# Kernel tuning notes

Measured on AMD Instinct MI355X. Metric: run time of the kernel, lower is better.

## Reference

```python
import jax, jax.numpy as jnp
import numpy as np

N_NODES = 50000
N_EDGES = 600000
D_IN = 256    # hidden_lstm
D_GNN = 128   # hidden_gnn
D_OUT = 1     # out_channels


def setup_inputs() -> dict:
    key = jax.random.key(0)
    ks = jax.random.split(key, 8)
    x = jax.random.normal(ks[0], (N_NODES, D_IN), dtype=jnp.float32)
    edge_index = jax.random.randint(ks[1], (2, N_EDGES), 0, N_NODES, dtype=jnp.int32)
    # SAGEConv params: lin_l applied to aggregated neighbors (with bias), lin_r to root
    s_in = 1.0 / np.sqrt(D_IN)
    W_l = jax.random.uniform(ks[2], (D_IN, D_GNN), jnp.float32, -s_in, s_in)
    b_l = jax.random.uniform(ks[3], (D_GNN,), jnp.float32, -s_in, s_in)
    W_r = jax.random.uniform(ks[4], (D_IN, D_GNN), jnp.float32, -s_in, s_in)
    # fc head
    s_g = 1.0 / np.sqrt(D_GNN)
    W_fc = jax.random.uniform(ks[5], (D_GNN, D_OUT), jnp.float32, -s_g, s_g)
    b_fc = jax.random.uniform(ks[6], (D_OUT,), jnp.float32, -s_g, s_g)
    return {"x": x, "edge_index": edge_index, "W_l": W_l, "b_l": b_l,
            "W_r": W_r, "W_fc": W_fc, "b_fc": b_fc}


def reference(x, edge_index, W_l, b_l, W_r, W_fc, b_fc):
    # SAGEConv, aggr='mean': out = lin_l(mean_{j in N(i)} x_j) + lin_r(x_i)
    src = edge_index[0]  # message source
    dst = edge_index[1]  # message target
    n = x.shape[0]
    agg = jax.ops.segment_sum(x[src], dst, num_segments=n)            # [N, D_IN]
    cnt = jax.ops.segment_sum(jnp.ones((src.shape[0], 1), x.dtype), dst,
                              num_segments=n)                         # [N, 1]
    mean = agg / jnp.maximum(cnt, 1.0)
    h = mean @ W_l + b_l + x @ W_r                                    # [N, D_GNN]
    pred = jax.nn.sigmoid(h @ W_fc + b_fc).squeeze()                  # [N]
    return h, pred
```

## Files before the change

kernel.cpp:

```cpp
#include <hip/hip_runtime.h>
#include <hip/hip_bf16.h>
#include <math.h>

#define N_NODES 50000
#define N_EDGES 600000
#define D_IN 256
#define D_GNN 128
#define CAP 32
#define MAX_OVER 8192
#define EB_STRIDE 264

typedef short s16x8 __attribute__((ext_vector_type(8)));
typedef float f32x4 __attribute__((ext_vector_type(4)));

__device__ __forceinline__ unsigned short f2bf(float f) {
  unsigned int u = __float_as_uint(f);
  u += 0x7FFFu + ((u >> 16) & 1u);
  return (unsigned short)(u >> 16);
}

__global__ __launch_bounds__(256) void pack0(
    const float* __restrict__ Wl, const float* __restrict__ Wr,
    ushort* __restrict__ Wcp, int* __restrict__ cursor,
    int* __restrict__ ovcnt) {
  int i = blockIdx.x * 256 + threadIdx.x;
  if (i < N_NODES) cursor[i] = 0;
  if (i == 0) ovcnt[0] = 0;
  if (i < 8192) {
    int q = i & 3, col = (i >> 2) & 255, ks = i >> 10;
    const float* W = (col < 128) ? Wl : Wr;
    int c = col & 127;
    int k0 = ks * 32 + q * 8;
    s16x8 v;
#pragma unroll
    for (int j = 0; j < 8; j++) v[j] = (short)f2bf(W[(k0 + j) * D_GNN + c]);
    *((s16x8*)(Wcp + (size_t)i * 8)) = v;
  }
}

__global__ __launch_bounds__(256, 6) void fused_gemm_fill(
    const float* __restrict__ x, const ushort* __restrict__ Wcp,
    const float* __restrict__ b_l, const int* __restrict__ ei,
    int* __restrict__ cursor, ushort* __restrict__ colp,
    int* __restrict__ ovcnt, int2* __restrict__ over,
    ushort* __restrict__ yb, ushort* __restrict__ yrb) {
  __shared__ ushort eb[16 * EB_STRIDE];
  const int t = threadIdx.x;
  const int n0 = blockIdx.x * 16;
  const int l = t & 63;
  const int w = t >> 6;
  const int lq = l >> 4, l16 = l & 15;

  const int e = blockIdx.x * 256 + t;
  int esrc = 0, edst = 0;
  const bool has_e = (e < N_EDGES);
  if (has_e) {
    esrc = ei[e];
    edst = ei[N_EDGES + e];
  }

  int row = n0 + l16;
  if (row >= N_NODES) row = N_NODES - 1;
  const float* arow = x + (size_t)row * D_IN + lq * 8;

  const ushort* bptr[4];
#pragma unroll
  for (int ct = 0; ct < 4; ct++) {
    int col = w * 64 + ct * 16 + l16;
    bptr[ct] = Wcp + ((size_t)col * 4 + lq) * 8;
  }

  f32x4 acc[4];
#pragma unroll
  for (int ct = 0; ct < 4; ct++) acc[ct] = (f32x4){0.f, 0.f, 0.f, 0.f};

#pragma unroll
  for (int ks = 0; ks < 8; ks++) {
    float4 a0 = *((const float4*)(arow + ks * 32));
    float4 a1 = *((const float4*)(arow + ks * 32 + 4));
    union { s16x8 v; ushort4 u[2]; } ua;
    __hip_bfloat162 h0 = __float22bfloat162_rn(make_float2(a0.x, a0.y));
    __hip_bfloat162 h1 = __float22bfloat162_rn(make_float2(a0.z, a0.w));
    __hip_bfloat162 h2 = __float22bfloat162_rn(make_float2(a1.x, a1.y));
    __hip_bfloat162 h3 = __float22bfloat162_rn(make_float2(a1.z, a1.w));
    ua.u[0].x = ((ushort2*)&h0)->x; ua.u[0].y = ((ushort2*)&h0)->y;
    ua.u[0].z = ((ushort2*)&h1)->x; ua.u[0].w = ((ushort2*)&h1)->y;
    ua.u[1].x = ((ushort2*)&h2)->x; ua.u[1].y = ((ushort2*)&h2)->y;
    ua.u[1].z = ((ushort2*)&h3)->x; ua.u[1].w = ((ushort2*)&h3)->y;
    s16x8 A = ua.v;
#pragma unroll
    for (int ct = 0; ct < 4; ct++) {
      s16x8 B = *((const s16x8*)(bptr[ct] + (size_t)ks * 8192));
      acc[ct] = __builtin_amdgcn_mfma_f32_16x16x32_bf16(A, B, acc[ct], 0, 0, 0);
    }
  }

  int pos = -1;
  if (has_e) pos = atomicAdd(&cursor[edst], 1);

#pragma unroll
  for (int ct = 0; ct < 4; ct++) {
    int col = w * 64 + ct * 16 + l16;
    float bias = (col >= 128) ? b_l[col - 128] : 0.f;
#pragma unroll
    for (int r = 0; r < 4; r++) {
      eb[(lq * 4 + r) * EB_STRIDE + col] = f2bf(acc[ct][r] + bias);
    }
  }

  if (pos >= 0) {
    if (pos < CAP) {
      colp[edst * CAP + pos] = (ushort)esrc;
    } else {
      int o = atomicAdd(ovcnt, 1);
      if (o < MAX_OVER) over[o] = make_int2(edst, esrc);
    }
  }

  __syncthreads();

#pragma unroll
  for (int p = 0; p < 2; p++) {
    int id = p * 256 + t;
    int rl = id >> 5;
    int c8 = (id & 31) * 8;
    int gn = n0 + rl;
    if (gn < N_NODES) {
      s16x8 v = *((const s16x8*)(eb + rl * EB_STRIDE + c8));
      if (c8 < 128)
        *((s16x8*)(yb + (size_t)gn * D_GNN + c8)) = v;
      else
        *((s16x8*)(yrb + (size_t)gn * D_GNN + (c8 - 128))) = v;
    }
  }
}

__global__ __launch_bounds__(256) void gather_pred(
    const int* __restrict__ cursor, const ushort* __restrict__ colp,
    const int* __restrict__ ovcnt, const int2* __restrict__ over,
    const ushort* __restrict__ yb, const ushort* __restrict__ yrb,
    const float* __restrict__ Wfc, const float* __restrict__ bfc,
    float* __restrict__ h, float* __restrict__ pred) {
  const int node = (blockIdx.x * 256 + threadIdx.x) >> 6;
  const int lane = threadIdx.x & 63;
  if (node >= N_NODES) return;
  const int degt = cursor[node];
  const int m = min(degt, CAP);
  float ax = 0.f, ay = 0.f;
  const unsigned int* y32 = (const unsigned int*)yb;

  int c = (lane < m) ? (int)colp[node * CAP + lane] : 0;
  int j = 0;
  for (; j + 4 <= m; j += 4) {
    int s0 = __shfl(c, j), s1 = __shfl(c, j + 1);
    int s2 = __shfl(c, j + 2), s3 = __shfl(c, j + 3);
    unsigned int v0 = y32[(size_t)s0 * 64 + lane];
    unsigned int v1 = y32[(size_t)s1 * 64 + lane];
    unsigned int v2 = y32[(size_t)s2 * 64 + lane];
    unsigned int v3 = y32[(size_t)s3 * 64 + lane];
    ax += __uint_as_float(v0 << 16) + __uint_as_float(v1 << 16) +
          __uint_as_float(v2 << 16) + __uint_as_float(v3 << 16);
    ay += __uint_as_float(v0 & 0xFFFF0000u) + __uint_as_float(v1 & 0xFFFF0000u) +
          __uint_as_float(v2 & 0xFFFF0000u) + __uint_as_float(v3 & 0xFFFF0000u);
  }
  for (; j < m; j++) {
    int s0 = __shfl(c, j);
    unsigned int v0 = y32[(size_t)s0 * 64 + lane];
    ax += __uint_as_float(v0 << 16);
    ay += __uint_as_float(v0 & 0xFFFF0000u);
  }
  if (degt > CAP) {
    int nov = min(ovcnt[0], MAX_OVER);
    for (int k = 0; k < nov; k++) {
      int2 ov = over[k];
      if (ov.x == node) {
        unsigned int v0 = y32[(size_t)ov.y * 64 + lane];
        ax += __uint_as_float(v0 << 16);
        ay += __uint_as_float(v0 & 0xFFFF0000u);
      }
    }
  }

  const float ic = degt > 0 ? 1.f / (float)degt : 0.f;
  unsigned int yrv = ((const unsigned int*)yrb)[(size_t)node * 64 + lane];
  float h0 = ax * ic + __uint_as_float(yrv << 16);
  float h1 = ay * ic + __uint_as_float(yrv & 0xFFFF0000u);
  float2 hv; hv.x = h0; hv.y = h1;
  ((float2*)h)[(size_t)node * 64 + lane] = hv;
  float s = h0 * Wfc[2 * lane] + h1 * Wfc[2 * lane + 1];
#pragma unroll
  for (int off = 32; off > 0; off >>= 1) s += __shfl_down(s, off);
  if (lane == 0) pred[node] = 1.f / (1.f + expf(-(s + bfc[0])));
}

extern "C" void kernel_launch(void* const* d_in, const int* in_sizes, int n_in,
                              void* d_out, int out_size, void* d_ws,
                              size_t ws_size, hipStream_t stream) {
  const float* x   = (const float*)d_in[0];
  const int*   ei  = (const int*)d_in[1];
  const float* Wl  = (const float*)d_in[2];
  const float* bl  = (const float*)d_in[3];
  const float* Wr  = (const float*)d_in[4];
  const float* Wfc = (const float*)d_in[5];
  const float* bfc = (const float*)d_in[6];

  float* out  = (float*)d_out;
  float* h    = out;
  float* pred = out + (size_t)N_NODES * D_GNN;

  ushort* Wcp   = (ushort*)d_ws;
  ushort* yb    = Wcp + 8192 * 8;
  ushort* yrb   = yb + (size_t)N_NODES * D_GNN;
  int*   cursor = (int*)(yrb + (size_t)N_NODES * D_GNN);
  int*   ovcnt  = cursor + N_NODES;
  int2*  over   = (int2*)(ovcnt + 1);
  ushort* colp  = (ushort*)(over + MAX_OVER);

  pack0<<<(N_NODES + 255) / 256, 256, 0, stream>>>(Wl, Wr, Wcp, cursor, ovcnt);

  fused_gemm_fill<<<(N_NODES + 15) / 16, 256, 0, stream>>>(
      x, Wcp, bl, ei, cursor, colp, ovcnt, over, yb, yrb);

  gather_pred<<<(N_NODES * 64 + 255) / 256, 256, 0, stream>>>(
      cursor, colp, ovcnt, over, yb, yrb, Wfc, bfc, h, pred);
}
```

Measured before the change: 192.9 us.

## Make fused GEMM/fill kernel persistent with register-resident weights

Converts the fused GEMM and CSR-fill kernel into a persistent grid of 512 blocks that first grid-strides over edges to do the atomic bucket fill, then loops over 16-row node tiles. Each wave loads its 64-column slice of the packed bf16 weights into registers once and reuses them across all tiles, and prefetches the whole A row slice into registers before the MFMAs. This removes the repeated per-block weight loads, but costs a large register footprint (launch bounds drop to 2 blocks per CU), adds two barriers per tile, and gives up overlap between the edge atomics and the GEMM.

New measurement: 203.2 us. +5.3%, slower.

```diff
diff --git a/kernel.cpp b/kernel.cpp
--- a/kernel.cpp
+++ b/kernel.cpp
@@ -8,6 +8,8 @@
 #define D_GNN 128
 #define CAP 32
 #define MAX_OVER 8192
+#define NBLK 512
+#define NTILES 3125
 #define EB_STRIDE 264
 
 typedef short s16x8 __attribute__((ext_vector_type(8)));
@@ -38,7 +40,7 @@
   }
 }
 
-__global__ __launch_bounds__(256, 6) void fused_gemm_fill(
+__global__ __launch_bounds__(256, 2) void fused_gemm_fill(
     const float* __restrict__ x, const ushort* __restrict__ Wcp,
     const float* __restrict__ b_l, const int* __restrict__ ei,
     int* __restrict__ cursor, ushort* __restrict__ colp,
@@ -46,69 +48,14 @@
     ushort* __restrict__ yb, ushort* __restrict__ yrb) {
   __shared__ ushort eb[16 * EB_STRIDE];
   const int t = threadIdx.x;
-  const int n0 = blockIdx.x * 16;
   const int l = t & 63;
   const int w = t >> 6;
   const int lq = l >> 4, l16 = l & 15;
 
-  const int e = blockIdx.x * 256 + t;
-  int esrc = 0, edst = 0;
-  const bool has_e = (e < N_EDGES);
-  if (has_e) {
-    esrc = ei[e];
-    edst = ei[N_EDGES + e];
-  }
-
-  int row = n0 + l16;
-  if (row >= N_NODES) row = N_NODES - 1;
-  const float* arow = x + (size_t)row * D_IN + lq * 8;
-
-  const ushort* bptr[4];
-#pragma unroll
-  for (int ct = 0; ct < 4; ct++) {
-    int col = w * 64 + ct * 16 + l16;
-    bptr[ct] = Wcp + ((size_t)col * 4 + lq) * 8;
-  }
-
-  f32x4 acc[4];
-#pragma unroll
-  for (int ct = 0; ct < 4; ct++) acc[ct] = (f32x4){0.f, 0.f, 0.f, 0.f};
-
-#pragma unroll
-  for (int ks = 0; ks < 8; ks++) {
-    float4 a0 = *((const float4*)(arow + ks * 32));
-    float4 a1 = *((const float4*)(arow + ks * 32 + 4));
-    union { s16x8 v; ushort4 u[2]; } ua;
-    __hip_bfloat162 h0 = __float22bfloat162_rn(make_float2(a0.x, a0.y));
-    __hip_bfloat162 h1 = __float22bfloat162_rn(make_float2(a0.z, a0.w));
-    __hip_bfloat162 h2 = __float22bfloat162_rn(make_float2(a1.x, a1.y));
-    __hip_bfloat162 h3 = __float22bfloat162_rn(make_float2(a1.z, a1.w));
-    ua.u[0].x = ((ushort2*)&h0)->x; ua.u[0].y = ((ushort2*)&h0)->y;
-    ua.u[0].z = ((ushort2*)&h1)->x; ua.u[0].w = ((ushort2*)&h1)->y;
-    ua.u[1].x = ((ushort2*)&h2)->x; ua.u[1].y = ((ushort2*)&h2)->y;
-    ua.u[1].z = ((ushort2*)&h3)->x; ua.u[1].w = ((ushort2*)&h3)->y;
-    s16x8 A = ua.v;
-#pragma unroll
-    for (int ct = 0; ct < 4; ct++) {
-      s16x8 B = *((const s16x8*)(bptr[ct] + (size_t)ks * 8192));
-      acc[ct] = __builtin_amdgcn_mfma_f32_16x16x32_bf16(A, B, acc[ct], 0, 0, 0);
-    }
-  }
-
-  int pos = -1;
-  if (has_e) pos = atomicAdd(&cursor[edst], 1);
-
-#pragma unroll
-  for (int ct = 0; ct < 4; ct++) {
-    int col = w * 64 + ct * 16 + l16;
-    float bias = (col >= 128) ? b_l[col - 128] : 0.f;
-#pragma unroll
-    for (int r = 0; r < 4; r++) {
-      eb[(lq * 4 + r) * EB_STRIDE + col] = f2bf(acc[ct][r] + bias);
-    }
-  }
-
-  if (pos >= 0) {
+  for (int e = blockIdx.x * 256 + t; e < N_EDGES; e += NBLK * 256) {
+    int esrc = ei[e];
+    int edst = ei[N_EDGES + e];
+    int pos = atomicAdd(&cursor[edst], 1);
     if (pos < CAP) {
       colp[edst * CAP + pos] = (ushort)esrc;
     } else {
@@ -117,21 +64,72 @@
     }
   }
 
-  __syncthreads();
-
-#pragma unroll
-  for (int p = 0; p < 2; p++) {
-    int id = p * 256 + t;
-    int rl = id >> 5;
-    int c8 = (id & 31) * 8;
-    int gn = n0 + rl;
-    if (gn < N_NODES) {
+  const int c0 = w * 64;
+  s16x8 Breg[4][8];
+  float bias[4];
+#pragma unroll
+  for (int ct = 0; ct < 4; ct++) {
+    int col = c0 + ct * 16 + l16;
+    const ushort* bp = Wcp + ((size_t)col * 4 + lq) * 8;
+#pragma unroll
+    for (int ks = 0; ks < 8; ks++)
+      Breg[ct][ks] = *((const s16x8*)(bp + (size_t)ks * 8192));
+    bias[ct] = (col >= 128) ? b_l[col - 128] : 0.f;
+  }
+
+  for (int tt = blockIdx.x; tt < NTILES; tt += NBLK) {
+    const int n0 = tt * 16;
+    const float* ap = x + (size_t)(n0 + l16) * D_IN + lq * 8;
+
+    float4 av[16];
+#pragma unroll
+    for (int k2 = 0; k2 < 16; k2++)
+      av[k2] = *((const float4*)(ap + (k2 >> 1) * 32 + (k2 & 1) * 4));
+
+    f32x4 acc[4];
+#pragma unroll
+    for (int ct = 0; ct < 4; ct++) acc[ct] = (f32x4){0.f, 0.f, 0.f, 0.f};
+
+#pragma unroll
+    for (int ks = 0; ks < 8; ks++) {
+      float4 a0 = av[2 * ks], a1 = av[2 * ks + 1];
+      union { s16x8 v; ushort4 u[2]; } ua;
+      __hip_bfloat162 h0 = __float22bfloat162_rn(make_float2(a0.x, a0.y));
+      __hip_bfloat162 h1 = __float22bfloat162_rn(make_float2(a0.z, a0.w));
+      __hip_bfloat162 h2 = __float22bfloat162_rn(make_float2(a1.x, a1.y));
+      __hip_bfloat162 h3 = __float22bfloat162_rn(make_float2(a1.z, a1.w));
+      ua.u[0].x = ((ushort2*)&h0)->x; ua.u[0].y = ((ushort2*)&h0)->y;
+      ua.u[0].z = ((ushort2*)&h1)->x; ua.u[0].w = ((ushort2*)&h1)->y;
+      ua.u[1].x = ((ushort2*)&h2)->x; ua.u[1].y = ((ushort2*)&h2)->y;
+      ua.u[1].z = ((ushort2*)&h3)->x; ua.u[1].w = ((ushort2*)&h3)->y;
+      s16x8 A = ua.v;
+#pragma unroll
+      for (int ct = 0; ct < 4; ct++)
+        acc[ct] = __builtin_amdgcn_mfma_f32_16x16x32_bf16(
+            A, Breg[ct][ks], acc[ct], 0, 0, 0);
+    }
+
+#pragma unroll
+    for (int ct = 0; ct < 4; ct++) {
+      int col = c0 + ct * 16 + l16;
+#pragma unroll
+      for (int r = 0; r < 4; r++)
+        eb[(lq * 4 + r) * EB_STRIDE + col] = f2bf(acc[ct][r] + bias[ct]);
+    }
+    __syncthreads();
+#pragma unroll
+    for (int p = 0; p < 2; p++) {
+      int id = p * 256 + t;
+      int rl = id >> 5;
+      int c8 = (id & 31) * 8;
       s16x8 v = *((const s16x8*)(eb + rl * EB_STRIDE + c8));
+      int gn = n0 + rl;
       if (c8 < 128)
         *((s16x8*)(yb + (size_t)gn * D_GNN + c8)) = v;
       else
         *((s16x8*)(yrb + (size_t)gn * D_GNN + (c8 - 128))) = v;
     }
+    __syncthreads();
   }
 }
 
@@ -218,7 +216,7 @@
 
   pack0<<<(N_NODES + 255) / 256, 256, 0, stream>>>(Wl, Wr, Wcp, cursor, ovcnt);
 
-  fused_gemm_fill<<<(N_NODES + 15) / 16, 256, 0, stream>>>(
+  fused_gemm_fill<<<NBLK, 256, 0, stream>>>(
       x, Wcp, bl, ei, cursor, colp, ovcnt, over, yb, yrb);
 
   gather_pred<<<(N_NODES * 64 + 255) / 256, 256, 0, stream>>>(
```
